# Optimization experiments

Hardware: AMD Instinct MI355X
Metric: run time of the kernel (lower is better)

## Reference

```python
import jax, jax.numpy as jnp
import numpy as np

N, E, G = 50000, 800000, 64   # nodes, edges, graphs in batch
H, C = 4, 64                  # GAT heads, per-head channels (concat=False -> averaged)
F_IN, D_OUT = 16, 32
NEG_SLOPE = 0.2


def setup_inputs():
    key = jax.random.key(0)
    ks = jax.random.split(key, 20)
    s = 0.05
    inp = {
        "x": jax.random.normal(ks[0], (N, F_IN), jnp.float32),
        "edge_index": jax.random.randint(ks[1], (2, E), 0, N, dtype=jnp.int32),
        "batch": jnp.sort(jax.random.randint(ks[2], (N,), 0, G, dtype=jnp.int32)),
        "Wp": jax.random.normal(ks[3], (F_IN, H * C // H), jnp.float32) * s,  # 16 -> 64
        "bp": jnp.zeros((64,), jnp.float32),
        "Wo": jax.random.normal(ks[4], (64, D_OUT), jnp.float32) * s,
        "bo": jnp.zeros((D_OUT,), jnp.float32),
    }
    for l in range(3):
        inp[f"W{l}"] = jax.random.normal(ks[5 + 3 * l], (64, H * C), jnp.float32) * s
        inp[f"as{l}"] = jax.random.normal(ks[6 + 3 * l], (H, C), jnp.float32) * s
        inp[f"ad{l}"] = jax.random.normal(ks[7 + 3 * l], (H, C), jnp.float32) * s
        inp[f"b{l}"] = jnp.zeros((C,), jnp.float32)
    return inp


def _gat_layer(h, src, dst, W, a_src, a_dst, b):
    # h: [N, 64] -> per-head features [N, H, C]
    hw = (h @ W).reshape(N, H, C)
    # per-node attention logits [N, H]
    al_s = jnp.sum(hw * a_src, axis=-1)
    al_d = jnp.sum(hw * a_dst, axis=-1)
    # per-edge logits (src contributes alpha_src, dst contributes alpha_dst)
    e = jax.nn.leaky_relu(al_s[src] + al_d[dst], NEG_SLOPE)  # [Et, H]
    # neighbor-wise softmax over edges grouped by destination node
    emax = jax.ops.segment_max(e, dst, num_segments=N)
    ex = jnp.exp(e - emax[dst])
    denom = jax.ops.segment_sum(ex, dst, num_segments=N)
    alpha = ex / denom[dst]                                   # [Et, H]
    # weighted scatter-add of source features to destinations
    msg = alpha[:, :, None] * hw[src]                         # [Et, H, C]
    out = jax.ops.segment_sum(msg, dst, num_segments=N)       # [N, H, C]
    return out.mean(axis=1) + b                               # concat=False: head mean


def reference(x, edge_index, batch, Wp, bp, W0, as0, ad0, b0,
              W1, as1, ad1, b1, W2, as2, ad2, b2, Wo, bo):
    # add self-loops once (PyG GATConv default add_self_loops=True)
    loop = jnp.arange(N, dtype=edge_index.dtype)
    src = jnp.concatenate([edge_index[0], loop])
    dst = jnp.concatenate([edge_index[1], loop])

    h = jax.nn.relu(x @ Wp + bp)
    for (W, a_s, a_d, b) in ((W0, as0, ad0, b0), (W1, as1, ad1, b1), (W2, as2, ad2, b2)):
        h = jax.nn.relu(_gat_layer(h, src, dst, W, a_s, a_d, b))

    # global mean pool over graphs
    sums = jax.ops.segment_sum(h, batch, num_segments=G)
    cnt = jax.ops.segment_sum(jnp.ones((N,), h.dtype), batch, num_segments=G)
    pooled = sums / jnp.maximum(cnt, 1.0)[:, None]
    return pooled @ Wo + bo
```

## Files before the change

kernel.cpp:

```cpp
#include <hip/hip_runtime.h>

#define NEG_SLOPE 0.2f

typedef __attribute__((ext_vector_type(8))) short bf16x8;
typedef __attribute__((ext_vector_type(4))) float f32x4;

__device__ __forceinline__ float lrelu(float x) { return fmaxf(x, NEG_SLOPE * x); }

__device__ __forceinline__ float bf2f(unsigned short u) {
  return __uint_as_float(((unsigned int)u) << 16);
}
__device__ __forceinline__ unsigned short f2bf(float f) {
  unsigned int u = __float_as_uint(f);
  u += 0x7fffu + ((u >> 16) & 1u);
  return (unsigned short)(u >> 16);
}

__global__ void proj_kernel(const float* __restrict__ x, const float* __restrict__ Wp,
                            const float* __restrict__ bp, unsigned short* __restrict__ h,
                            int n_nodes) {
  int idx = blockIdx.x * blockDim.x + threadIdx.x;
  int n = idx >> 6, c = idx & 63;
  if (n >= n_nodes) return;
  float acc = bp[c];
#pragma unroll
  for (int k = 0; k < 16; ++k) acc += x[n * 16 + k] * Wp[k * 64 + c];
  h[n * 64 + c] = f2bf(fmaxf(acc, 0.f));
}

__global__ void hist_kernel(const int* __restrict__ dst, int* __restrict__ deg, int e) {
  int i = blockIdx.x * blockDim.x + threadIdx.x;
  if (i < e) atomicAdd(&deg[dst[i]], 1);
}

__global__ __launch_bounds__(256) void scan_a(const int* __restrict__ deg, int* __restrict__ rowp,
                                              int* __restrict__ bsum, int n) {
  __shared__ int s[256];
  int t = threadIdx.x;
  int base = blockIdx.x * 1024 + t * 4;
  int d0 = (base + 0 < n) ? deg[base + 0] + 1 : 0;
  int d1 = (base + 1 < n) ? deg[base + 1] + 1 : 0;
  int d2 = (base + 2 < n) ? deg[base + 2] + 1 : 0;
  int d3 = (base + 3 < n) ? deg[base + 3] + 1 : 0;
  s[t] = d0 + d1 + d2 + d3;
  __syncthreads();
  for (int off = 1; off < 256; off <<= 1) {
    int v = 0;
    if (t >= off) v = s[t - off];
    __syncthreads();
    if (t >= off) s[t] += v;
    __syncthreads();
  }
  int p = (t == 0) ? 0 : s[t - 1];
  if (base + 0 < n) rowp[base + 0] = p;
  p += d0;
  if (base + 1 < n) rowp[base + 1] = p;
  p += d1;
  if (base + 2 < n) rowp[base + 2] = p;
  p += d2;
  if (base + 3 < n) rowp[base + 3] = p;
  if (t == 255) bsum[blockIdx.x] = s[255];
}

__global__ void scan_b(const int* __restrict__ bsum, int* __restrict__ bpre, int nb) {
  int t = threadIdx.x;
  int v = (t < nb) ? bsum[t] : 0;
  int orig = v;
#pragma unroll
  for (int off = 1; off < 64; off <<= 1) {
    int u = __shfl_up(v, off);
    if (t >= off) v += u;
  }
  bpre[t] = v - orig;
  if (t == 63) bpre[64] = v;
}

__global__ void scan_c(int* __restrict__ rowp, const int* __restrict__ bpre,
                       int* __restrict__ cnt, int* __restrict__ col, int n) {
  int i = blockIdx.x * blockDim.x + threadIdx.x;
  if (i < n) {
    int r = rowp[i] + bpre[i >> 10];
    rowp[i] = r;
    cnt[i] = 1;
    col[r] = i;
  }
  if (i == 0) rowp[n] = bpre[64];
}

__global__ void scatter_kernel(const int* __restrict__ src, const int* __restrict__ dst,
                               const int* __restrict__ rowp, int* __restrict__ cnt,
                               int* __restrict__ col, int e) {
  int i = blockIdx.x * blockDim.x + threadIdx.x;
  if (i < e) {
    int d = dst[i];
    int pos = rowp[d] + atomicAdd(&cnt[d], 1);
    col[pos] = src[i];
  }
}

__global__ void prep_wa3(const float* __restrict__ W0, const float* __restrict__ as0, const float* __restrict__ ad0,
                         const float* __restrict__ W1, const float* __restrict__ as1, const float* __restrict__ ad1,
                         const float* __restrict__ W2, const float* __restrict__ as2, const float* __restrict__ ad2,
                         float* __restrict__ Wa) {
  int l = blockIdx.x;
  const float* W  = l == 0 ? W0  : l == 1 ? W1  : W2;
  const float* as = l == 0 ? as0 : l == 1 ? as1 : as2;
  const float* ad = l == 0 ? ad0 : l == 1 ? ad1 : ad2;
  int t = threadIdx.x;
  int k = t >> 2, h = t & 3;
  float ss = 0.f, sd = 0.f;
  for (int c = 0; c < 64; ++c) {
    float w = W[k * 256 + h * 64 + c];
    ss += w * as[h * 64 + c];
    sd += w * ad[h * 64 + c];
  }
  Wa[l * 512 + k * 8 + h] = ss;
  Wa[l * 512 + k * 8 + 4 + h] = sd;
}

__global__ void prep_wsw(const float* __restrict__ W0, const float* __restrict__ W1,
                         const float* __restrict__ W2, const float* __restrict__ Wa,
                         unsigned short* __restrict__ Wsw, unsigned short* __restrict__ Wasw) {
  int l = blockIdx.x;
  const float* W = l == 0 ? W0 : l == 1 ? W1 : W2;
  int t = threadIdx.x;
  for (int s = t; s < 2048; s += 256) {
    int nt = s >> 7, kk = (s >> 6) & 1, lane = s & 63;
    int kq = lane >> 4, r = lane & 15;
#pragma unroll
    for (int j = 0; j < 8; ++j) {
      int k = kk * 32 + kq * 8 + j;
      Wsw[(size_t)l * 16384 + (size_t)s * 8 + j] = f2bf(W[k * 256 + nt * 16 + r]);
    }
  }
  if (t < 128) {
    int lane = t & 63, kq = lane >> 4, r = lane & 15;
    int kk = t >> 6;
#pragma unroll
    for (int j = 0; j < 8; ++j) {
      int k = kk * 32 + kq * 8 + j;
      float v = (r < 8) ? Wa[l * 512 + k * 8 + r] : 0.f;
      Wasw[l * 1024 + t * 8 + j] = f2bf(v);
    }
  }
}

__global__ __launch_bounds__(256) void hw_kernel(const unsigned short* __restrict__ hb,
                                                 const unsigned short* __restrict__ Wsw,
                                                 const unsigned short* __restrict__ Wasw,
                                                 unsigned short* __restrict__ hwb,
                                                 float* __restrict__ al_s, float* __restrict__ al_d,
                                                 int n_nodes) {
  int t = threadIdx.x;
  int w = t >> 6, lane = t & 63;
  int kq = lane >> 4, r16 = lane & 15;
  int n0 = blockIdx.x << 6;

  bf16x8 a[4][2];
#pragma unroll
  for (int m = 0; m < 4; ++m) {
    int row = min(n0 + m * 16 + r16, n_nodes - 1);
    const unsigned short* p = hb + (size_t)row * 64 + kq * 8;
    a[m][0] = *(const bf16x8*)(p);
    a[m][1] = *(const bf16x8*)(p + 32);
  }
  bf16x8 b[4][2];
#pragma unroll
  for (int nt = 0; nt < 4; ++nt) {
    int ntg = w * 4 + nt;
    const unsigned short* p = Wsw + ((size_t)ntg * 128 + lane) * 8;
    b[nt][0] = *(const bf16x8*)(p);
    b[nt][1] = *(const bf16x8*)(p + 512);
  }

  f32x4 acc[4][4];
#pragma unroll
  for (int m = 0; m < 4; ++m)
#pragma unroll
    for (int nt = 0; nt < 4; ++nt) acc[m][nt] = (f32x4){0.f, 0.f, 0.f, 0.f};

#pragma unroll
  for (int m = 0; m < 4; ++m)
#pragma unroll
    for (int nt = 0; nt < 4; ++nt) {
      acc[m][nt] = __builtin_amdgcn_mfma_f32_16x16x32_bf16(a[m][0], b[nt][0], acc[m][nt], 0, 0, 0);
      acc[m][nt] = __builtin_amdgcn_mfma_f32_16x16x32_bf16(a[m][1], b[nt][1], acc[m][nt], 0, 0, 0);
    }

#pragma unroll
  for (int m = 0; m < 4; ++m) {
#pragma unroll
    for (int j = 0; j < 4; ++j) {
      int row = n0 + m * 16 + kq * 4 + j;
      if (row < n_nodes) {
#pragma unroll
        for (int nt = 0; nt < 4; ++nt) {
          int col = (w * 4 + nt) * 16 + r16;
          hwb[(size_t)row * 256 + col] = f2bf(acc[m][nt][j]);
        }
      }
    }
  }

  bf16x8 ba0 = *(const bf16x8*)(Wasw + lane * 8);
  bf16x8 ba1 = *(const bf16x8*)(Wasw + (64 + lane) * 8);
  f32x4 accl = (f32x4){0.f, 0.f, 0.f, 0.f};
  accl = __builtin_amdgcn_mfma_f32_16x16x32_bf16(a[w][0], ba0, accl, 0, 0, 0);
  accl = __builtin_amdgcn_mfma_f32_16x16x32_bf16(a[w][1], ba1, accl, 0, 0, 0);
  if (r16 < 8) {
#pragma unroll
    for (int j = 0; j < 4; ++j) {
      int row = n0 + w * 16 + kq * 4 + j;
      if (row < n_nodes) {
        if (r16 < 4) al_s[row * 4 + r16] = accl[j];
        else         al_d[row * 4 + (r16 - 4)] = accl[j];
      }
    }
  }
}

__global__ __launch_bounds__(256) void gat_agg(const int* __restrict__ rowp, const int* __restrict__ col,
                                               const float* __restrict__ alS, const float* __restrict__ alD,
                                               const unsigned short* __restrict__ hwb,
                                               const float* __restrict__ bias,
                                               unsigned short* __restrict__ hout,
                                               int n_nodes) {
  __shared__ uint2 pw[4][64 * 4];
  int t = threadIdx.x;
  int wslot = t >> 6, lane = t & 63;
  int node = blockIdx.x * 4 + wslot;
  if (node >= n_nodes) return;
  int base = rowp[node];
  int degv = rowp[node + 1] - base;
  int head = lane >> 4;
  unsigned int laneoff = (unsigned int)lane << 3;
  float4 ald4 = *(const float4*)(alD + (size_t)node * 4);

  float a0 = 0.f, a1 = 0.f, a2 = 0.f, a3 = 0.f, denom = 0.f;

  for (int c0 = 0; c0 < degv; c0 += 64) {
    int cnt = min(64, degv - c0);
    if (lane < cnt) {
      int s = col[base + c0 + lane];
      float4 as4 = *(const float4*)(alS + (size_t)s * 4);
      unsigned int ab = (unsigned int)s << 9;
      float w0 = __expf(lrelu(as4.x + ald4.x));
      float w1 = __expf(lrelu(as4.y + ald4.y));
      float w2 = __expf(lrelu(as4.z + ald4.z));
      float w3 = __expf(lrelu(as4.w + ald4.w));
      pw[wslot][lane * 4 + 0] = make_uint2(ab, __float_as_uint(w0));
      pw[wslot][lane * 4 + 1] = make_uint2(ab, __float_as_uint(w1));
      pw[wslot][lane * 4 + 2] = make_uint2(ab, __float_as_uint(w2));
      pw[wslot][lane * 4 + 3] = make_uint2(ab, __float_as_uint(w3));
    }
#pragma unroll 4
    for (int i = 0; i < cnt; ++i) {
      uint2 p = pw[wslot][i * 4 + head];
      float w = __uint_as_float(p.y);
      uint2 v = *(const uint2*)((const char*)hwb + (p.x + laneoff));
      denom += w;
      a0 += w * __uint_as_float(v.x << 16);
      a1 += w * __uint_as_float(v.x & 0xffff0000u);
      a2 += w * __uint_as_float(v.y << 16);
      a3 += w * __uint_as_float(v.y & 0xffff0000u);
    }
  }

  float inv = 1.f / denom;
  a0 *= inv; a1 *= inv; a2 *= inv; a3 *= inv;

  a0 += __shfl_xor(a0, 16); a0 += __shfl_xor(a0, 32);
  a1 += __shfl_xor(a1, 16); a1 += __shfl_xor(a1, 32);
  a2 += __shfl_xor(a2, 16); a2 += __shfl_xor(a2, 32);
  a3 += __shfl_xor(a3, 16); a3 += __shfl_xor(a3, 32);

  if (lane < 16) {
    float4 b = *(const float4*)(bias + lane * 4);
    ushort4 o;
    o.x = f2bf(fmaxf(0.25f * a0 + b.x, 0.f));
    o.y = f2bf(fmaxf(0.25f * a1 + b.y, 0.f));
    o.z = f2bf(fmaxf(0.25f * a2 + b.z, 0.f));
    o.w = f2bf(fmaxf(0.25f * a3 + b.w, 0.f));
    *(ushort4*)(hout + (size_t)node * 64 + lane * 4) = o;
  }
}

__global__ void pool_kernel(const unsigned short* __restrict__ h, const int* __restrict__ batch,
                            float* __restrict__ pool, float* __restrict__ pcnt, int n_nodes) {
  int c = threadIdx.x;
  int n0 = blockIdx.x * 64;
  int n1 = min(n0 + 64, n_nodes);
  float acc = 0.f;
  int run = 0;
  int gcur = batch[n0];
  for (int n = n0; n < n1; ++n) {
    int g = batch[n];
    if (g != gcur) {
      atomicAdd(&pool[gcur * 64 + c], acc);
      if (c == 0) atomicAdd(&pcnt[gcur], (float)run);
      acc = 0.f; run = 0; gcur = g;
    }
    acc += bf2f(h[(size_t)n * 64 + c]);
    ++run;
  }
  atomicAdd(&pool[gcur * 64 + c], acc);
  if (c == 0) atomicAdd(&pcnt[gcur], (float)run);
}

__global__ void out_kernel(const float* __restrict__ pool, const float* __restrict__ pcnt,
                           const float* __restrict__ Wo, const float* __restrict__ bo,
                           float* __restrict__ out, int g_total) {
  int idx = blockIdx.x * blockDim.x + threadIdx.x;
  if (idx >= g_total * 32) return;
  int g = idx >> 5, d = idx & 31;
  float inv = 1.f / fmaxf(pcnt[g], 1.f);
  float acc = bo[d];
#pragma unroll
  for (int c = 0; c < 64; ++c) acc += (pool[g * 64 + c] * inv) * Wo[c * 32 + d];
  out[idx] = acc;
}

extern "C" void kernel_launch(void* const* d_in, const int* in_sizes, int n_in,
                              void* d_out, int out_size, void* d_ws, size_t ws_size,
                              hipStream_t stream) {
  const float* x     = (const float*)d_in[0];
  const int*   ei    = (const int*)d_in[1];
  const int*   batch = (const int*)d_in[2];
  const float* Wp    = (const float*)d_in[3];
  const float* bp    = (const float*)d_in[4];
  const float* Wo    = (const float*)d_in[5];
  const float* bo    = (const float*)d_in[6];
  const float* Wl[3]  = {(const float*)d_in[7],  (const float*)d_in[11], (const float*)d_in[15]};
  const float* Asl[3] = {(const float*)d_in[8],  (const float*)d_in[12], (const float*)d_in[16]};
  const float* Adl[3] = {(const float*)d_in[9],  (const float*)d_in[13], (const float*)d_in[17]};
  const float* Bl[3]  = {(const float*)d_in[10], (const float*)d_in[14], (const float*)d_in[18]};

  const int N = in_sizes[0] / 16;
  const int E = in_sizes[1] / 2;
  const int G = out_size / 32;
  const int Et = E + N;
  const int* src = ei;
  const int* dst = ei + E;
  const int NB = (N + 1023) / 1024;

  char* ws = (char*)d_ws;
  size_t off = 0;
  auto take = [&](size_t bytes) -> void* {
    void* p = ws + off;
    off = (off + bytes + 255) & ~(size_t)255;
    return p;
  };
  unsigned short* h_a = (unsigned short*)take((size_t)N * 64 * 2);
  unsigned short* h_b = (unsigned short*)take((size_t)N * 64 * 2);
  unsigned short* hwb = (unsigned short*)take((size_t)N * 256 * 2);
  float* alS   = (float*)take((size_t)N * 4 * 4);
  float* alD   = (float*)take((size_t)N * 4 * 4);
  int*   deg   = (int*)take((size_t)N * 4);
  int*   cnt   = (int*)take((size_t)N * 4);
  int*   rowp  = (int*)take((size_t)(N + 1) * 4);
  int*   col   = (int*)take((size_t)Et * 4);
  int*   bsum  = (int*)take((size_t)64 * 4);
  int*   bpre  = (int*)take((size_t)65 * 4);
  float* Wa    = (float*)take((size_t)3 * 512 * 4);
  unsigned short* Wsw  = (unsigned short*)take((size_t)3 * 16384 * 2);
  unsigned short* Wasw = (unsigned short*)take((size_t)3 * 1024 * 2);
  float* pool  = (float*)take((size_t)G * 64 * 4);
  float* pcnt  = (float*)take((size_t)G * 4);
  (void)ws_size; (void)n_in;

  prep_wa3<<<3, 256, 0, stream>>>(Wl[0], Asl[0], Adl[0], Wl[1], Asl[1], Adl[1],
                                  Wl[2], Asl[2], Adl[2], Wa);
  prep_wsw<<<3, 256, 0, stream>>>(Wl[0], Wl[1], Wl[2], Wa, Wsw, Wasw);

  hipMemsetAsync(deg, 0, (size_t)N * 4, stream);
  hist_kernel<<<(E + 255) / 256, 256, 0, stream>>>(dst, deg, E);
  scan_a<<<NB, 256, 0, stream>>>(deg, rowp, bsum, N);
  scan_b<<<1, 64, 0, stream>>>(bsum, bpre, NB);
  scan_c<<<(N + 255) / 256, 256, 0, stream>>>(rowp, bpre, cnt, col, N);
  scatter_kernel<<<(E + 255) / 256, 256, 0, stream>>>(src, dst, rowp, cnt, col, E);

  proj_kernel<<<((size_t)N * 64 + 255) / 256, 256, 0, stream>>>(x, Wp, bp, h_a, N);

  const unsigned short* hin = h_a;
  unsigned short* hout = h_b;
  for (int l = 0; l < 3; ++l) {
    hw_kernel<<<(N + 63) / 64, 256, 0, stream>>>(hin, Wsw + (size_t)l * 16384,
                                                 Wasw + (size_t)l * 1024, hwb, alS, alD, N);
    gat_agg<<<(N + 3) / 4, 256, 0, stream>>>(rowp, col, alS, alD, hwb, Bl[l], hout, N);
    const unsigned short* tmp = hout;
    hout = (unsigned short*)hin;
    hin = tmp;
  }

  hipMemsetAsync(pool, 0, (size_t)G * 64 * 4, stream);
  hipMemsetAsync(pcnt, 0, (size_t)G * 4, stream);
  pool_kernel<<<(N + 63) / 64, 64, 0, stream>>>(hin, batch, pool, pcnt, N);
  out_kernel<<<(G * 32 + 255) / 256, 256, 0, stream>>>(pool, pcnt, Wo, bo, (float*)d_out, G);
}
```

Measured before the change: 413.3 us.

## Process two edges per wavefront with 16-byte gathers; fuse prep kernels and memsets

The GAT aggregation now splits each wavefront into two halves that handle alternate edges. Each lane gathers 8 bf16 features with a 16-byte load instead of 4 with 8 bytes, and the two halves are merged with a cross-half shuffle. This halves the serial inner-loop trip count per node and widens the memory transactions, at the cost of more registers. Separately, the two weight-prep kernels are fused into one that keeps the attention vectors in shared memory, and the two pool memsets are merged into one, cutting launch overhead.

Result: no change. 410.4 us (-0.7%).

```diff
diff --git a/kernel.cpp b/kernel.cpp
--- a/kernel.cpp
+++ b/kernel.cpp
@@ -98,32 +98,29 @@
   }
 }
 
-__global__ void prep_wa3(const float* __restrict__ W0, const float* __restrict__ as0, const float* __restrict__ ad0,
-                         const float* __restrict__ W1, const float* __restrict__ as1, const float* __restrict__ ad1,
-                         const float* __restrict__ W2, const float* __restrict__ as2, const float* __restrict__ ad2,
-                         float* __restrict__ Wa) {
+__global__ __launch_bounds__(256) void prep_kernel(
+    const float* __restrict__ W0, const float* __restrict__ as0, const float* __restrict__ ad0,
+    const float* __restrict__ W1, const float* __restrict__ as1, const float* __restrict__ ad1,
+    const float* __restrict__ W2, const float* __restrict__ as2, const float* __restrict__ ad2,
+    unsigned short* __restrict__ Wsw, unsigned short* __restrict__ Wasw) {
+  __shared__ float wa[512];
   int l = blockIdx.x;
   const float* W  = l == 0 ? W0  : l == 1 ? W1  : W2;
   const float* as = l == 0 ? as0 : l == 1 ? as1 : as2;
   const float* ad = l == 0 ? ad0 : l == 1 ? ad1 : ad2;
   int t = threadIdx.x;
-  int k = t >> 2, h = t & 3;
-  float ss = 0.f, sd = 0.f;
-  for (int c = 0; c < 64; ++c) {
-    float w = W[k * 256 + h * 64 + c];
-    ss += w * as[h * 64 + c];
-    sd += w * ad[h * 64 + c];
-  }
-  Wa[l * 512 + k * 8 + h] = ss;
-  Wa[l * 512 + k * 8 + 4 + h] = sd;
-}
-
-__global__ void prep_wsw(const float* __restrict__ W0, const float* __restrict__ W1,
-                         const float* __restrict__ W2, const float* __restrict__ Wa,
-                         unsigned short* __restrict__ Wsw, unsigned short* __restrict__ Wasw) {
-  int l = blockIdx.x;
-  const float* W = l == 0 ? W0 : l == 1 ? W1 : W2;
-  int t = threadIdx.x;
+  {
+    int k = t >> 2, h = t & 3;
+    float ss = 0.f, sd = 0.f;
+    for (int c = 0; c < 64; ++c) {
+      float w = W[k * 256 + h * 64 + c];
+      ss += w * as[h * 64 + c];
+      sd += w * ad[h * 64 + c];
+    }
+    wa[k * 8 + h] = ss;
+    wa[k * 8 + 4 + h] = sd;
+  }
+  __syncthreads();
   for (int s = t; s < 2048; s += 256) {
     int nt = s >> 7, kk = (s >> 6) & 1, lane = s & 63;
     int kq = lane >> 4, r = lane & 15;
@@ -139,7 +136,7 @@
 #pragma unroll
     for (int j = 0; j < 8; ++j) {
       int k = kk * 32 + kq * 8 + j;
-      float v = (r < 8) ? Wa[l * 512 + k * 8 + r] : 0.f;
+      float v = (r < 8) ? wa[k * 8 + r] : 0.f;
       Wasw[l * 1024 + t * 8 + j] = f2bf(v);
     }
   }
@@ -232,56 +229,86 @@
   if (node >= n_nodes) return;
   int base = rowp[node];
   int degv = rowp[node + 1] - base;
-  int head = lane >> 4;
-  unsigned int laneoff = (unsigned int)lane << 3;
+  int l31 = lane & 31;
+  int half = lane >> 5;
+  int headw = l31 >> 3;
+  unsigned int laneoff = (unsigned int)l31 << 4;
   float4 ald4 = *(const float4*)(alD + (size_t)node * 4);
 
-  float a0 = 0.f, a1 = 0.f, a2 = 0.f, a3 = 0.f, denom = 0.f;
+  float a0 = 0.f, a1 = 0.f, a2 = 0.f, a3 = 0.f;
+  float a4 = 0.f, a5 = 0.f, a6 = 0.f, a7 = 0.f, denom = 0.f;
 
   for (int c0 = 0; c0 < degv; c0 += 64) {
     int cnt = min(64, degv - c0);
-    if (lane < cnt) {
-      int s = col[base + c0 + lane];
-      float4 as4 = *(const float4*)(alS + (size_t)s * 4);
-      unsigned int ab = (unsigned int)s << 9;
-      float w0 = __expf(lrelu(as4.x + ald4.x));
-      float w1 = __expf(lrelu(as4.y + ald4.y));
-      float w2 = __expf(lrelu(as4.z + ald4.z));
-      float w3 = __expf(lrelu(as4.w + ald4.w));
-      pw[wslot][lane * 4 + 0] = make_uint2(ab, __float_as_uint(w0));
-      pw[wslot][lane * 4 + 1] = make_uint2(ab, __float_as_uint(w1));
-      pw[wslot][lane * 4 + 2] = make_uint2(ab, __float_as_uint(w2));
-      pw[wslot][lane * 4 + 3] = make_uint2(ab, __float_as_uint(w3));
-    }
+    {
+      unsigned int ab = 0u;
+      float w0 = 0.f, w1 = 0.f, w2 = 0.f, w3 = 0.f;
+      if (lane < cnt) {
+        int s = col[base + c0 + lane];
+        float4 as4 = *(const float4*)(alS + (size_t)s * 4);
+        ab = (unsigned int)s << 9;
+        w0 = __expf(lrelu(as4.x + ald4.x));
+        w1 = __expf(lrelu(as4.y + ald4.y));
+        w2 = __expf(lrelu(as4.z + ald4.z));
+        w3 = __expf(lrelu(as4.w + ald4.w));
+      }
+      uint4* pd = (uint4*)&pw[wslot][lane * 4];
+      pd[0] = make_uint4(ab, __float_as_uint(w0), ab, __float_as_uint(w1));
+      pd[1] = make_uint4(ab, __float_as_uint(w2), ab, __float_as_uint(w3));
+    }
+    int iters = (cnt + 1) >> 1;
 #pragma unroll 4
-    for (int i = 0; i < cnt; ++i) {
-      uint2 p = pw[wslot][i * 4 + head];
+    for (int i = 0; i < iters; ++i) {
+      int e = i * 2 + half;
+      uint2 p = pw[wslot][e * 4 + headw];
       float w = __uint_as_float(p.y);
-      uint2 v = *(const uint2*)((const char*)hwb + (p.x + laneoff));
+      uint4 v = *(const uint4*)((const char*)hwb + (p.x + laneoff));
       denom += w;
       a0 += w * __uint_as_float(v.x << 16);
       a1 += w * __uint_as_float(v.x & 0xffff0000u);
       a2 += w * __uint_as_float(v.y << 16);
       a3 += w * __uint_as_float(v.y & 0xffff0000u);
-    }
-  }
-
+      a4 += w * __uint_as_float(v.z << 16);
+      a5 += w * __uint_as_float(v.z & 0xffff0000u);
+      a6 += w * __uint_as_float(v.w << 16);
+      a7 += w * __uint_as_float(v.w & 0xffff0000u);
+    }
+  }
+
+  denom += __shfl_xor(denom, 32);
+  a0 += __shfl_xor(a0, 32); a1 += __shfl_xor(a1, 32);
+  a2 += __shfl_xor(a2, 32); a3 += __shfl_xor(a3, 32);
+  a4 += __shfl_xor(a4, 32); a5 += __shfl_xor(a5, 32);
+  a6 += __shfl_xor(a6, 32); a7 += __shfl_xor(a7, 32);
   float inv = 1.f / denom;
   a0 *= inv; a1 *= inv; a2 *= inv; a3 *= inv;
-
-  a0 += __shfl_xor(a0, 16); a0 += __shfl_xor(a0, 32);
-  a1 += __shfl_xor(a1, 16); a1 += __shfl_xor(a1, 32);
-  a2 += __shfl_xor(a2, 16); a2 += __shfl_xor(a2, 32);
-  a3 += __shfl_xor(a3, 16); a3 += __shfl_xor(a3, 32);
-
-  if (lane < 16) {
-    float4 b = *(const float4*)(bias + lane * 4);
-    ushort4 o;
-    o.x = f2bf(fmaxf(0.25f * a0 + b.x, 0.f));
-    o.y = f2bf(fmaxf(0.25f * a1 + b.y, 0.f));
-    o.z = f2bf(fmaxf(0.25f * a2 + b.z, 0.f));
-    o.w = f2bf(fmaxf(0.25f * a3 + b.w, 0.f));
-    *(ushort4*)(hout + (size_t)node * 64 + lane * 4) = o;
+  a4 *= inv; a5 *= inv; a6 *= inv; a7 *= inv;
+
+  a0 += __shfl_xor(a0, 8); a0 += __shfl_xor(a0, 16);
+  a1 += __shfl_xor(a1, 8); a1 += __shfl_xor(a1, 16);
+  a2 += __shfl_xor(a2, 8); a2 += __shfl_xor(a2, 16);
+  a3 += __shfl_xor(a3, 8); a3 += __shfl_xor(a3, 16);
+  a4 += __shfl_xor(a4, 8); a4 += __shfl_xor(a4, 16);
+  a5 += __shfl_xor(a5, 8); a5 += __shfl_xor(a5, 16);
+  a6 += __shfl_xor(a6, 8); a6 += __shfl_xor(a6, 16);
+  a7 += __shfl_xor(a7, 8); a7 += __shfl_xor(a7, 16);
+
+  if (lane < 8) {
+    const float* bp = bias + lane * 8;
+    float4 b0 = *(const float4*)(bp);
+    float4 b1 = *(const float4*)(bp + 4);
+    ushort4 o0, o1;
+    o0.x = f2bf(fmaxf(0.25f * a0 + b0.x, 0.f));
+    o0.y = f2bf(fmaxf(0.25f * a1 + b0.y, 0.f));
+    o0.z = f2bf(fmaxf(0.25f * a2 + b0.z, 0.f));
+    o0.w = f2bf(fmaxf(0.25f * a3 + b0.w, 0.f));
+    o1.x = f2bf(fmaxf(0.25f * a4 + b1.x, 0.f));
+    o1.y = f2bf(fmaxf(0.25f * a5 + b1.y, 0.f));
+    o1.z = f2bf(fmaxf(0.25f * a6 + b1.z, 0.f));
+    o1.w = f2bf(fmaxf(0.25f * a7 + b1.w, 0.f));
+    unsigned short* op = hout + (size_t)node * 64 + lane * 8;
+    *(ushort4*)(op) = o0;
+    *(ushort4*)(op + 4) = o1;
   }
 }
 
@@ -361,16 +388,14 @@
   int*   col   = (int*)take((size_t)Et * 4);
   int*   bsum  = (int*)take((size_t)64 * 4);
   int*   bpre  = (int*)take((size_t)65 * 4);
-  float* Wa    = (float*)take((size_t)3 * 512 * 4);
   unsigned short* Wsw  = (unsigned short*)take((size_t)3 * 16384 * 2);
   unsigned short* Wasw = (unsigned short*)take((size_t)3 * 1024 * 2);
   float* pool  = (float*)take((size_t)G * 64 * 4);
   float* pcnt  = (float*)take((size_t)G * 4);
   (void)ws_size; (void)n_in;
 
-  prep_wa3<<<3, 256, 0, stream>>>(Wl[0], Asl[0], Adl[0], Wl[1], Asl[1], Adl[1],
-                                  Wl[2], Asl[2], Adl[2], Wa);
-  prep_wsw<<<3, 256, 0, stream>>>(Wl[0], Wl[1], Wl[2], Wa, Wsw, Wasw);
+  prep_kernel<<<3, 256, 0, stream>>>(Wl[0], Asl[0], Adl[0], Wl[1], Asl[1], Adl[1],
+                                     Wl[2], Asl[2], Adl[2], Wsw, Wasw);
 
   hipMemsetAsync(deg, 0, (size_t)N * 4, stream);
   hist_kernel<<<(E + 255) / 256, 256, 0, stream>>>(dst, deg, E);
@@ -392,8 +417,7 @@
     hin = tmp;
   }
 
-  hipMemsetAsync(pool, 0, (size_t)G * 64 * 4, stream);
-  hipMemsetAsync(pcnt, 0, (size_t)G * 4, stream);
+  hipMemsetAsync(pool, 0, (size_t)((char*)(pcnt + G) - (char*)pool), stream);
   pool_kernel<<<(N + 63) / 64, 64, 0, stream>>>(hin, batch, pool, pcnt, N);
   out_kernel<<<(G * 32 + 255) / 256, 256, 0, stream>>>(pool, pcnt, Wo, bo, (float*)d_out, G);
 }
```
